# Performance work log

Measured on AMD Instinct MI355X. Metric: run time of the kernel, lower is better.

The kernel has to match this reference:

```python
import jax, jax.numpy as jnp
import numpy as np

B, E, H, V, KV = 64, 256, 512, 50257, 2048


def setup_inputs() -> dict:
    key = jax.random.key(0)
    ks = jax.random.split(key, 16)
    s_e = 1.0 / np.sqrt(E)
    s_h = 1.0 / np.sqrt(H)
    s_eh = 1.0 / np.sqrt(E + H)
    return {
        "input": jax.random.randint(ks[0], (B,), 0, V),
        "h0": jax.random.normal(ks[1], (B, H), jnp.float32),
        "c0": jax.random.normal(ks[2], (B, H), jnp.float32),
        "k": jax.random.normal(ks[3], (KV, E), jnp.float32),
        "context_vector": jax.random.normal(ks[4], (B, H), jnp.float32),
        # embedding table
        "embedding": jax.random.normal(ks[5], (V, E), jnp.float32) * 0.02,
        # LSTMCell params (PyTorch layout: gates ordered i,f,g,o)
        "W_ih": jax.random.uniform(ks[6], (4 * H, E), jnp.float32, -s_h, s_h),
        "b_ih": jax.random.uniform(ks[7], (4 * H,), jnp.float32, -s_h, s_h),
        "W_hh": jax.random.uniform(ks[8], (4 * H, H), jnp.float32, -s_h, s_h),
        "b_hh": jax.random.uniform(ks[9], (4 * H,), jnp.float32, -s_h, s_h),
        # attn_key MLP: Linear(E+H,E) -> tanh -> Linear(E,E) -> tanh -> Linear(E,1)
        "W1": jax.random.uniform(ks[10], (E, E + H), jnp.float32, -s_eh, s_eh),
        "b1": jnp.zeros((E,), jnp.float32),
        "W2": jax.random.uniform(ks[11], (E, E), jnp.float32, -s_e, s_e),
        "b2": jnp.zeros((E,), jnp.float32),
        "W3": jax.random.uniform(ks[12], (1, E), jnp.float32, -s_e, s_e),
        "b3": jnp.zeros((1,), jnp.float32),
        # output projection Linear(H, V)
        "W_out": jax.random.uniform(ks[13], (V, H), jnp.float32, -s_h, s_h),
        "b_out": jax.random.uniform(ks[14], (V,), jnp.float32, -s_h, s_h),
    }


def reference(input, h0, c0, k, context_vector, embedding, W_ih, b_ih, W_hh, b_hh,
              W1, b1, W2, b2, W3, b3, W_out, b_out):
    # embedding lookup (dropout in eval mode = identity)
    x = embedding[input]  # (B, E)
    # LSTMCell
    gates = x @ W_ih.T + b_ih + h0 @ W_hh.T + b_hh  # (B, 4H)
    i, f, g, o = jnp.split(gates, 4, axis=-1)
    i = jax.nn.sigmoid(i)
    f = jax.nn.sigmoid(f)
    g = jnp.tanh(g)
    o = jax.nn.sigmoid(o)
    c_t = f * c0 + i * g
    h_t = o * jnp.tanh(c_t)  # (B, H)
    # key attention: broadcast h_t over kv keys, keys over batch (torch.cat-repeat in original)
    h_b = jnp.broadcast_to(h_t[:, None, :], (B, KV, H))
    k_b = jnp.broadcast_to(k[None, :, :], (B, KV, E))
    feat = jnp.concatenate([h_b, k_b], axis=-1)  # (B, KV, H+E)
    u = jnp.tanh(feat @ W1.T + b1)
    u = jnp.tanh(u @ W2.T + b2)
    scores = (u @ W3.T + b3)[..., 0]  # (B, KV)
    # vocab logits; original pads V-KV zeros in front then adds -> scores hit last KV slots
    o_t = h_t @ W_out.T + b_out  # (B, V)
    o_t = o_t.at[:, V - KV:].add(scores)
    y_t = jax.nn.log_softmax(o_t, axis=-1)
    return (y_t, h_t, c_t)
```

## Files before the change

kernel.cpp:

```cpp
#include <hip/hip_runtime.h>
#include <math.h>

namespace {

constexpr int B = 64, E = 256, H = 512, V = 50257, KV = 2048;
constexpr int NOUT = (V + 63) / 64;
constexpr int PSTRIDE = 800;

typedef __bf16 bf16x8 __attribute__((ext_vector_type(8)));
typedef float f32x4 __attribute__((ext_vector_type(4)));

__device__ __forceinline__ float fast_tanh(float x) {
  float e = __expf(2.f * x);
  return 1.f - 2.f / (e + 1.f);
}
__device__ __forceinline__ float sigmoidf(float x) {
  return 1.f / (1.f + __expf(-x));
}
__device__ __forceinline__ f32x4 mfma16(bf16x8 a, bf16x8 b, f32x4 c) {
  return __builtin_amdgcn_mfma_f32_16x16x32_bf16(a, b, c, 0, 0, 0);
}

__global__ __launch_bounds__(256) void k_gates(const int* __restrict__ inp,
    const float* __restrict__ h0, const float* __restrict__ emb,
    const float* __restrict__ W_ih, const float* __restrict__ b_ih,
    const float* __restrict__ W_hh, const float* __restrict__ b_hh,
    float* __restrict__ gates) {
  int b = threadIdx.x & 63;
  int j = blockIdx.x * 4 + (threadIdx.x >> 6);
  j = __builtin_amdgcn_readfirstlane(j);
  int row = inp[b];
  const float* xr = emb + (long)row * E;
  const float* wi = W_ih + (long)j * E;
  const float* hr = h0 + b * H;
  const float* wh = W_hh + (long)j * H;
  float acc = b_ih[j] + b_hh[j];
#pragma unroll 8
  for (int t = 0; t < E / 4; ++t) {
    float4 x4 = ((const float4*)xr)[t];
    float4 w4 = ((const float4*)wi)[t];
    acc += x4.x * w4.x + x4.y * w4.y + x4.z * w4.z + x4.w * w4.w;
  }
#pragma unroll 8
  for (int t = 0; t < H / 4; ++t) {
    float4 h4 = ((const float4*)hr)[t];
    float4 w4 = ((const float4*)wh)[t];
    acc += h4.x * w4.x + h4.y * w4.y + h4.z * w4.z + h4.w * w4.w;
  }
  gates[j * B + b] = acc;
}

__global__ __launch_bounds__(256) void k_lstm(const float* __restrict__ gates,
    const float* __restrict__ c0, float* __restrict__ out_h, float* __restrict__ out_c,
    __bf16* __restrict__ hp) {
  int i = blockIdx.x * 256 + threadIdx.x;
  int b = i >> 9, hh = i & 511;
  float gi = gates[(hh)*B + b];
  float gf = gates[(hh + 512) * B + b];
  float gg = gates[(hh + 1024) * B + b];
  float go = gates[(hh + 1536) * B + b];
  float c = sigmoidf(gf) * c0[i] + sigmoidf(gi) * fast_tanh(gg);
  float h = sigmoidf(go) * fast_tanh(c);
  out_h[i] = h;
  out_c[i] = c;
  hp[((hh >> 3) * 64 + b) * 8 + (hh & 7)] = (__bf16)h;
}

__global__ __launch_bounds__(256) void k_prep(const float* __restrict__ h_t,
    const float* __restrict__ W1, const float* __restrict__ b1,
    const float* __restrict__ k, const float* __restrict__ W2,
    float* __restrict__ Ah, float* __restrict__ Kp, __bf16* __restrict__ W2p) {
  __shared__ float ks_[64][257];
  int bid = blockIdx.x;
  int t = threadIdx.x;
  if (bid < 64) {
    int b = t & 63;
    int e = bid * 4 + (t >> 6);
    e = __builtin_amdgcn_readfirstlane(e);
    const float* hr = h_t + b * H;
    const float* wr = W1 + (long)e * (E + H);
    float acc = b1[e];
#pragma unroll 8
    for (int q = 0; q < H / 4; ++q) {
      float4 h4 = ((const float4*)hr)[q];
      float4 w4 = ((const float4*)wr)[q];
      acc += h4.x * w4.x + h4.y * w4.y + h4.z * w4.z + h4.w * w4.w;
    }
    Ah[b * E + e] = acc;
  } else if (bid < 192) {
    int t2 = bid - 64;
    int kv0 = (t2 & 31) * 64;
    int e0 = (t2 >> 5) * 64;
    for (int i = 0; i < 16; ++i) {
      int idx = i * 256 + t;
      int rr = idx >> 6, cc = (idx & 63) * 4;
      float4 v = *(const float4*)(k + (kv0 + rr) * E + cc);
      ks_[rr][cc] = v.x; ks_[rr][cc + 1] = v.y; ks_[rr][cc + 2] = v.z; ks_[rr][cc + 3] = v.w;
    }
    __syncthreads();
    int r0 = (t >> 4);
    int c0 = (t & 15) * 4;
    float acc[4][4] = {};
    const float* w0 = W1 + (long)(e0 + c0) * (E + H) + H;
    for (int kk = 0; kk < 256; kk += 4) {
      float4 w[4];
#pragma unroll
      for (int c = 0; c < 4; ++c) w[c] = *(const float4*)(w0 + (long)c * (E + H) + kk);
#pragma unroll
      for (int q = 0; q < 4; ++q) {
#pragma unroll
        for (int r = 0; r < 4; ++r) {
          float kvv = ks_[r0 + 16 * r][kk + q];
#pragma unroll
          for (int c = 0; c < 4; ++c) acc[r][c] += kvv * ((const float*)&w[c])[q];
        }
      }
    }
    for (int r = 0; r < 4; ++r)
      for (int c = 0; c < 4; ++c)
        Kp[(kv0 + r0 + 16 * r) * E + e0 + c0 + c] = acc[r][c];
  } else {
    int idx = (bid - 192) * 256 + t;
    int kk = idx >> 8, n = idx & 255;
    W2p[((kk >> 3) * 256 + n) * 8 + (kk & 7)] = (__bf16)W2[n * 256 + kk];
  }
}

__global__ __launch_bounds__(256) void k_attn(const float* __restrict__ Ah,
    const float* __restrict__ Kp, const __bf16* __restrict__ W2p,
    const float* __restrict__ b2, const float* __restrict__ W3, const float* __restrict__ b3,
    float* __restrict__ scoresT) {
  __shared__ __align__(16) unsigned char lds_[64 * 256 * 2];
  int tid = threadIdx.x;
  int blk = blockIdx.x;
  int b = blk >> 5;
  int kv0 = (blk & 31) * 64;
  for (int i = 0; i < 8; ++i) {
    int idx = i * 256 + tid;
    int row = idx >> 5;
    int k0 = (idx & 31) * 8;
    const float* ap = Ah + b * E + k0;
    const float* kp = Kp + (kv0 + row) * E + k0;
    float4 a0 = *(const float4*)ap;
    float4 a1 = *(const float4*)(ap + 4);
    float4 p0 = *(const float4*)kp;
    float4 p1 = *(const float4*)(kp + 4);
    bf16x8 u;
    u[0] = (__bf16)fast_tanh(a0.x + p0.x);
    u[1] = (__bf16)fast_tanh(a0.y + p0.y);
    u[2] = (__bf16)fast_tanh(a0.z + p0.z);
    u[3] = (__bf16)fast_tanh(a0.w + p0.w);
    u[4] = (__bf16)fast_tanh(a1.x + p1.x);
    u[5] = (__bf16)fast_tanh(a1.y + p1.y);
    u[6] = (__bf16)fast_tanh(a1.z + p1.z);
    u[7] = (__bf16)fast_tanh(a1.w + p1.w);
    int byte = (row * 512 + k0 * 2) ^ ((row & 7) << 4);
    *(bf16x8*)(lds_ + byte) = u;
  }
  __syncthreads();
  int l = tid & 63, wc = tid >> 6;
  int lr = l & 15, lg = l >> 4;
  float b2v[4], w3v[4];
#pragma unroll
  for (int nf = 0; nf < 4; ++nf) {
    int col = wc * 64 + nf * 16 + lr;
    b2v[nf] = b2[col];
    w3v[nf] = W3[col];
  }
  f32x4 acc[4][4] = {};
  for (int ks = 0; ks < 8; ++ks) {
    bf16x8 a[4], bf[4];
#pragma unroll
    for (int mf = 0; mf < 4; ++mf) {
      int row = mf * 16 + lr;
      int byte = (row * 512 + (ks * 32 + lg * 8) * 2) ^ ((row & 7) << 4);
      a[mf] = *(const bf16x8*)(lds_ + byte);
    }
#pragma unroll
    for (int nf = 0; nf < 4; ++nf) {
      int col = wc * 64 + nf * 16 + lr;
      bf[nf] = *(const bf16x8*)(W2p + ((ks * 4 + lg) * 256 + col) * 8);
    }
#pragma unroll
    for (int mf = 0; mf < 4; ++mf)
#pragma unroll
      for (int nf = 0; nf < 4; ++nf)
        acc[mf][nf] = mfma16(a[mf], bf[nf], acc[mf][nf]);
  }
  float p[4][4];
#pragma unroll
  for (int mf = 0; mf < 4; ++mf)
#pragma unroll
    for (int r = 0; r < 4; ++r) p[mf][r] = 0.f;
#pragma unroll
  for (int mf = 0; mf < 4; ++mf)
#pragma unroll
    for (int nf = 0; nf < 4; ++nf)
#pragma unroll
      for (int r = 0; r < 4; ++r) {
        float u2 = fast_tanh(acc[mf][nf][r] + b2v[nf]);
        p[mf][r] += u2 * w3v[nf];
      }
#pragma unroll
  for (int off = 1; off < 16; off <<= 1)
#pragma unroll
    for (int mf = 0; mf < 4; ++mf)
#pragma unroll
      for (int r = 0; r < 4; ++r) p[mf][r] += __shfl_xor(p[mf][r], off);
  __syncthreads();
  float* red = (float*)lds_;
  if (lr == 0) {
#pragma unroll
    for (int mf = 0; mf < 4; ++mf)
#pragma unroll
      for (int r = 0; r < 4; ++r) red[(mf * 16 + lg * 4 + r) * 4 + wc] = p[mf][r];
  }
  __syncthreads();
  if (tid < 64) {
    float s = red[tid * 4 + 0] + red[tid * 4 + 1] + red[tid * 4 + 2] + red[tid * 4 + 3] + b3[0];
    scoresT[(kv0 + tid) * 64 + b] = s;
  }
}

__global__ __launch_bounds__(256) void k_out(const __bf16* __restrict__ hp,
    const float* __restrict__ W_out, const float* __restrict__ b_out,
    const float* __restrict__ scoresT, float* __restrict__ o,
    float* __restrict__ pm, float* __restrict__ ps) {
  __shared__ float vbuf[64][65];
  __shared__ float rm[64][4], rs[64][4];
  int tid = threadIdx.x;
  int l = tid & 63, wn = tid >> 6;
  int lr = l & 15, lg = l >> 4;
  int col = blockIdx.x * 64 + wn * 16 + lr;
  int colc = col < V ? col : V - 1;
  const float* wr = W_out + (long)colc * H;
  f32x4 acc[4] = {};
  for (int ks = 0; ks < 16; ++ks) {
    bf16x8 a[4];
#pragma unroll
    for (int mf = 0; mf < 4; ++mf)
      a[mf] = *(const bf16x8*)(hp + ((ks * 4 + lg) * 64 + mf * 16 + lr) * 8);
    const float* wp = wr + ks * 32 + lg * 8;
    float4 w0 = *(const float4*)wp;
    float4 w1 = *(const float4*)(wp + 4);
    bf16x8 bf;
    bf[0] = (__bf16)w0.x; bf[1] = (__bf16)w0.y; bf[2] = (__bf16)w0.z; bf[3] = (__bf16)w0.w;
    bf[4] = (__bf16)w1.x; bf[5] = (__bf16)w1.y; bf[6] = (__bf16)w1.z; bf[7] = (__bf16)w1.w;
#pragma unroll
    for (int mf = 0; mf < 4; ++mf) acc[mf] = mfma16(a[mf], bf, acc[mf]);
  }
  bool valid = col < V;
  float bo = valid ? b_out[col] : 0.f;
  bool has = valid && col >= (V - KV);
  int scix = col - (V - KV);
#pragma unroll
  for (int mf = 0; mf < 4; ++mf)
#pragma unroll
    for (int r = 0; r < 4; ++r) {
      int m = mf * 16 + lg * 4 + r;
      float v = acc[mf][r] + bo;
      if (has) v += scoresT[scix * 64 + m];
      if (valid) o[(long)m * V + col] = v; else v = -1e30f;
      vbuf[m][wn * 16 + lr] = v;
    }
  __syncthreads();
  int row = tid & 63, g = tid >> 6;
  float mm = -1e30f;
#pragma unroll
  for (int c = 0; c < 16; ++c) mm = fmaxf(mm, vbuf[row][g * 16 + c]);
  float ssum = 0.f;
#pragma unroll
  for (int c = 0; c < 16; ++c) ssum += __expf(vbuf[row][g * 16 + c] - mm);
  rm[row][g] = mm; rs[row][g] = ssum;
  __syncthreads();
  if (tid < 64) {
    float M = fmaxf(fmaxf(rm[tid][0], rm[tid][1]), fmaxf(rm[tid][2], rm[tid][3]));
    float S = 0.f;
#pragma unroll
    for (int g2 = 0; g2 < 4; ++g2) S += rs[tid][g2] * __expf(rm[tid][g2] - M);
    pm[tid * PSTRIDE + blockIdx.x] = M;
    ps[tid * PSTRIDE + blockIdx.x] = S;
  }
}

__global__ __launch_bounds__(256) void k_z(const float* __restrict__ pm,
    const float* __restrict__ ps, float* __restrict__ logZ) {
  int r = blockIdx.x;
  int tid = threadIdx.x;
  float m = -1e30f, s = 0.f;
  for (int p = tid; p < NOUT; p += 256) {
    float om = pm[r * PSTRIDE + p];
    float os = ps[r * PSTRIDE + p];
    float M = fmaxf(m, om);
    s = s * __expf(m - M) + os * __expf(om - M);
    m = M;
  }
#pragma unroll
  for (int off = 1; off < 64; off <<= 1) {
    float om = __shfl_xor(m, off);
    float os = __shfl_xor(s, off);
    float M = fmaxf(m, om);
    s = s * __expf(m - M) + os * __expf(om - M);
    m = M;
  }
  __shared__ float sm[4], ss[4];
  int w = tid >> 6;
  if ((tid & 63) == 0) { sm[w] = m; ss[w] = s; }
  __syncthreads();
  if (tid == 0) {
    m = sm[0]; s = ss[0];
    for (int i = 1; i < 4; ++i) {
      float M = fmaxf(m, sm[i]);
      s = s * __expf(m - M) + ss[i] * __expf(sm[i] - M);
      m = M;
    }
    logZ[r] = m + __logf(s);
  }
}

__global__ __launch_bounds__(256) void k_sub(float* __restrict__ o, const float* __restrict__ logZ) {
  int r = blockIdx.y;
  float z = logZ[r];
  int i0 = (blockIdx.x * 256 + threadIdx.x) * 4;
  float* row = o + (long)r * V;
  if (i0 + 3 < V) {
    float4 v = *(float4*)(row + i0);
    v.x -= z; v.y -= z; v.z -= z; v.w -= z;
    *(float4*)(row + i0) = v;
  } else {
    for (int i = i0; i < V; ++i) row[i] -= z;
  }
}

}

extern "C" void kernel_launch(void* const* d_in, const int* in_sizes, int n_in,
                              void* d_out, int out_size, void* d_ws, size_t ws_size,
                              hipStream_t stream) {
  const int* inp = (const int*)d_in[0];
  const float* h0 = (const float*)d_in[1];
  const float* c0 = (const float*)d_in[2];
  const float* kk = (const float*)d_in[3];
  const float* emb = (const float*)d_in[5];
  const float* W_ih = (const float*)d_in[6];
  const float* b_ih = (const float*)d_in[7];
  const float* W_hh = (const float*)d_in[8];
  const float* b_hh = (const float*)d_in[9];
  const float* W1 = (const float*)d_in[10];
  const float* b1 = (const float*)d_in[11];
  const float* W2 = (const float*)d_in[12];
  const float* b2 = (const float*)d_in[13];
  const float* W3 = (const float*)d_in[14];
  const float* b3 = (const float*)d_in[15];
  const float* W_out = (const float*)d_in[16];
  const float* b_out = (const float*)d_in[17];

  float* y = (float*)d_out;
  float* h_t = y + (size_t)B * V;
  float* c_t = h_t + (size_t)B * H;

  char* ws = (char*)d_ws;
  float* gates = (float*)ws;                 ws += (size_t)4 * H * B * 4;
  float* Ah = (float*)ws;                    ws += (size_t)B * E * 4;
  float* Kp = (float*)ws;                    ws += (size_t)KV * E * 4;
  float* scoresT = (float*)ws;               ws += (size_t)B * KV * 4;
  float* logZ = (float*)ws;                  ws += 256;
  float* pm = (float*)ws;                    ws += (size_t)B * PSTRIDE * 4;
  float* ps = (float*)ws;                    ws += (size_t)B * PSTRIDE * 4;
  __bf16* W2p = (__bf16*)ws;                 ws += (size_t)E * E * 2;
  __bf16* hp = (__bf16*)ws;                  ws += (size_t)B * H * 2;

  hipLaunchKernelGGL(k_gates, dim3(4 * H / 4), dim3(256), 0, stream,
                     inp, h0, emb, W_ih, b_ih, W_hh, b_hh, gates);
  hipLaunchKernelGGL(k_lstm, dim3(B * H / 256), dim3(256), 0, stream, gates, c0, h_t, c_t, hp);
  hipLaunchKernelGGL(k_prep, dim3(448), dim3(256), 0, stream,
                     h_t, W1, b1, kk, W2, Ah, Kp, W2p);
  hipLaunchKernelGGL(k_attn, dim3(B * KV / 64), dim3(256), 0, stream,
                     Ah, Kp, W2p, b2, W3, b3, scoresT);
  hipLaunchKernelGGL(k_out, dim3(NOUT), dim3(256), 0, stream,
                     hp, W_out, b_out, scoresT, y, pm, ps);
  hipLaunchKernelGGL(k_z, dim3(B), dim3(256), 0, stream, pm, ps, logZ);
  hipLaunchKernelGGL(k_sub, dim3((V + 1023) / 1024, B), dim3(256), 0, stream, y, logZ);
}
```

Baseline: 169.8 us.

## Stage W_out tiles through swizzled LDS and coalesce logits stores

The output projection kernel now loads each block's 64 rows of W_out cooperatively with row-contiguous, coalesced reads. It converts them to bf16 and writes them into a 32 KB XOR-swizzled LDS buffer in two K-halves, and the MFMA B operands are read from there instead of strided per-lane global loads. The logits store is also rewritten to go through the LDS value buffer so that each row is written with contiguous columns rather than a scattered per-lane pattern. The trade-off is extra LDS usage and barriers per block, which may lower occupancy.

New measurement: 166.7 us. Within noise of the previous version (-1.8%).

```diff
diff --git a/kernel.cpp b/kernel.cpp
--- a/kernel.cpp
+++ b/kernel.cpp
@@ -226,29 +226,50 @@
     const float* __restrict__ W_out, const float* __restrict__ b_out,
     const float* __restrict__ scoresT, float* __restrict__ o,
     float* __restrict__ pm, float* __restrict__ ps) {
-  __shared__ float vbuf[64][65];
+  __shared__ __align__(16) unsigned char lds_[64 * 256 * 2];
   __shared__ float rm[64][4], rs[64][4];
   int tid = threadIdx.x;
   int l = tid & 63, wn = tid >> 6;
   int lr = l & 15, lg = l >> 4;
-  int col = blockIdx.x * 64 + wn * 16 + lr;
-  int colc = col < V ? col : V - 1;
-  const float* wr = W_out + (long)colc * H;
+  int col0 = blockIdx.x * 64;
   f32x4 acc[4] = {};
-  for (int ks = 0; ks < 16; ++ks) {
-    bf16x8 a[4];
-#pragma unroll
-    for (int mf = 0; mf < 4; ++mf)
-      a[mf] = *(const bf16x8*)(hp + ((ks * 4 + lg) * 64 + mf * 16 + lr) * 8);
-    const float* wp = wr + ks * 32 + lg * 8;
-    float4 w0 = *(const float4*)wp;
-    float4 w1 = *(const float4*)(wp + 4);
-    bf16x8 bf;
-    bf[0] = (__bf16)w0.x; bf[1] = (__bf16)w0.y; bf[2] = (__bf16)w0.z; bf[3] = (__bf16)w0.w;
-    bf[4] = (__bf16)w1.x; bf[5] = (__bf16)w1.y; bf[6] = (__bf16)w1.z; bf[7] = (__bf16)w1.w;
-#pragma unroll
-    for (int mf = 0; mf < 4; ++mf) acc[mf] = mfma16(a[mf], bf, acc[mf]);
-  }
+#pragma unroll
+  for (int hh = 0; hh < 2; ++hh) {
+    if (hh) __syncthreads();
+#pragma unroll
+    for (int i = 0; i < 8; ++i) {
+      int u = i * 256 + tid;
+      int row = u >> 5;
+      int c16 = u & 31;
+      int rr = col0 + row; if (rr > V - 1) rr = V - 1;
+      const float* p = W_out + (long)rr * H + hh * 256 + c16 * 8;
+      float4 w0 = *(const float4*)p;
+      float4 w1 = *(const float4*)(p + 4);
+      bf16x8 v;
+      v[0] = (__bf16)w0.x; v[1] = (__bf16)w0.y; v[2] = (__bf16)w0.z; v[3] = (__bf16)w0.w;
+      v[4] = (__bf16)w1.x; v[5] = (__bf16)w1.y; v[6] = (__bf16)w1.z; v[7] = (__bf16)w1.w;
+      int byte = (row * 512 + c16 * 16) ^ ((row & 7) << 4);
+      *(bf16x8*)(lds_ + byte) = v;
+    }
+    __syncthreads();
+    int r = wn * 16 + lr;
+    int rbase = r * 512;
+    int rsw = (r & 7) << 4;
+#pragma unroll
+    for (int ks2 = 0; ks2 < 8; ++ks2) {
+      int ksg = hh * 8 + ks2;
+      bf16x8 a[4];
+#pragma unroll
+      for (int mf = 0; mf < 4; ++mf)
+        a[mf] = *(const bf16x8*)(hp + ((ksg * 4 + lg) * 64 + mf * 16 + lr) * 8);
+      bf16x8 bv = *(const bf16x8*)(lds_ + ((rbase + ks2 * 64 + lg * 16) ^ rsw));
+#pragma unroll
+      for (int mf = 0; mf < 4; ++mf) acc[mf] = mfma16(a[mf], bv, acc[mf]);
+    }
+  }
+  __syncthreads();
+  float (*vbuf)[65] = (float(*)[65])lds_;
+  int col = col0 + wn * 16 + lr;
   bool valid = col < V;
   float bo = valid ? b_out[col] : 0.f;
   bool has = valid && col >= (V - KV);
@@ -260,10 +281,17 @@
       int m = mf * 16 + lg * 4 + r;
       float v = acc[mf][r] + bo;
       if (has) v += scoresT[scix * 64 + m];
-      if (valid) o[(long)m * V + col] = v; else v = -1e30f;
+      if (!valid) v = -1e30f;
       vbuf[m][wn * 16 + lr] = v;
     }
   __syncthreads();
+  int nvalid = V - col0; if (nvalid > 64) nvalid = 64;
+#pragma unroll
+  for (int i = 0; i < 16; ++i) {
+    int idx = i * 256 + tid;
+    int m = idx >> 6, c = idx & 63;
+    if (c < nvalid) o[(long)m * V + col0 + c] = vbuf[m][c];
+  }
   int row = tid & 63, g = tid >> 6;
   float mm = -1e30f;
 #pragma unroll
```
